# Optimization experiments

Measured on AMD Instinct MI355X. Metric: run time of the kernel, lower is better.

The kernel has to match this reference:

```python
import jax, jax.numpy as jnp
import numpy as np

EPS = 1e-12  # torch F.normalize eps

def setup_inputs() -> dict:
    key = jax.random.key(0)
    k1, k2 = jax.random.split(key)
    N, M, D = 256, 2000, 128
    gene_seq = jax.random.randint(k1, (N, M), 0, 4)
    embedding_mat = jax.random.normal(k2, (M, 4, D), dtype=jnp.float32) * (np.sqrt(2.0) / D)
    return {"gene_seq": gene_seq, "embedding_mat": embedding_mat}

def reference(gene_seq, embedding_mat):
    # L2-normalize each (gene, base) row along embedding dim (torch F.normalize semantics)
    norm = jnp.linalg.norm(embedding_mat, axis=-1, keepdims=True)
    table = embedding_mat / jnp.maximum(norm, EPS)  # (M, 4, D)
    M = table.shape[0]
    # One-hot einsum 'nmi,nmid->nmd' == direct gather of row gene_seq[n,m] at position m
    gene_idx = jnp.arange(M)[None, :]               # (1, M)
    out = table[gene_idx, gene_seq, :]              # (N, M, D)
    return out
```

## Files before the change

kernel.cpp:

```cpp
#include <hip/hip_runtime.h>


#define N_SEQ   256
#define M_GENES 2000
#define D_DIM   128
#define GENES_PER_BLOCK 8
#define N_CHUNK 64
#define GRID_X  (M_GENES / GENES_PER_BLOCK)
#define GRID_Y  (N_SEQ / N_CHUNK)

typedef float vfloat4 __attribute__((ext_vector_type(4)));

__global__ __launch_bounds__(256) void fused_gather_kernel(
    const int*   __restrict__ gene_seq,
    const float* __restrict__ emb,
    float*       __restrict__ out)
{
    const int tid  = threadIdx.x;
    const int wave = tid >> 6;
    const int lane = tid & 63;
    const int c    = lane & 31;

    const int m0    = blockIdx.x * GENES_PER_BLOCK;
    const int n0    = blockIdx.y * N_CHUNK;
    const int m_sel = m0 + (wave << 1) + (lane >> 5);

    vfloat4 r[4];
    #pragma unroll
    for (int g = 0; g < 4; ++g) {
        const vfloat4 v = *reinterpret_cast<const vfloat4*>(
            emb + (((m_sel << 2) + g) << 7) + (c << 2));
        float ss = v.x * v.x + v.y * v.y + v.z * v.z + v.w * v.w;
        ss += __shfl_xor(ss, 1, 32);
        ss += __shfl_xor(ss, 2, 32);
        ss += __shfl_xor(ss, 4, 32);
        ss += __shfl_xor(ss, 8, 32);
        ss += __shfl_xor(ss, 16, 32);
        const float inv = 1.0f / fmaxf(sqrtf(ss), 1e-12f);
        r[g] = v * inv;
    }

    const int g0 = gene_seq[(n0 + c)      * M_GENES + m_sel];
    const int g1 = gene_seq[(n0 + 32 + c) * M_GENES + m_sel];

    float* __restrict__ outbase = out + (size_t)(m_sel << 7) + (c << 2);

    #pragma unroll 4
    for (int n = 0; n < N_CHUNK; ++n) {
        const int src = (lane & 32) | (n & 31);
        const int gv  = __shfl((n < 32) ? g0 : g1, src, 64);

        const vfloat4 lo = (gv & 1) ? r[1] : r[0];
        const vfloat4 hi = (gv & 1) ? r[3] : r[2];
        const vfloat4 v  = (gv & 2) ? hi : lo;

        *reinterpret_cast<vfloat4*>(
            outbase + (size_t)(n0 + n) * (M_GENES * D_DIM)) = v;
    }
}

extern "C" void kernel_launch(void* const* d_in, const int* in_sizes, int n_in,
                              void* d_out, int out_size, void* d_ws, size_t ws_size,
                              hipStream_t stream) {
    const int*   gene_seq = (const int*)d_in[0];
    const float* emb      = (const float*)d_in[1];
    float*       out      = (float*)d_out;

    fused_gather_kernel<<<dim3(GRID_X, GRID_Y), dim3(256), 0, stream>>>(
        gene_seq, emb, out);
}
```

Measured before the change: 257.3 us.

## Stage normalized embedding tile and gene indices in LDS for gather

Each block now normalizes a 32-gene tile of embedding rows into shared memory and loads a 32x32 tile of gene indices with coalesced int2 reads. Output rows are then written from LDS using the index table, so each n-row writes 16KB contiguous spans per block instead of scattered 512B segments. It replaces register-held rows and per-element shuffles. In exchange it uses about 68KB of LDS per block, which limits occupancy, and it normalizes each embedding row once per n-chunk (8 times).

```diff
diff --git a/kernel.cpp b/kernel.cpp
--- a/kernel.cpp
+++ b/kernel.cpp
@@ -4,58 +4,82 @@
 #define N_SEQ   256
 #define M_GENES 2000
 #define D_DIM   128
-#define GENES_PER_BLOCK 8
-#define N_CHUNK 64
-#define GRID_X  (M_GENES / GENES_PER_BLOCK)
-#define GRID_Y  (N_SEQ / N_CHUNK)
+#define TILE_M  32
+#define N_TILES 63
+#define N_CHUNK 32
+#define NCH     (N_SEQ / N_CHUNK)
+#define THREADS 512
 
 typedef float vfloat4 __attribute__((ext_vector_type(4)));
 
-__global__ __launch_bounds__(256) void fused_gather_kernel(
+__global__ __launch_bounds__(THREADS) void gene_embed_kernel(
     const int*   __restrict__ gene_seq,
     const float* __restrict__ emb,
     float*       __restrict__ out)
 {
-    const int tid  = threadIdx.x;
-    const int wave = tid >> 6;
-    const int lane = tid & 63;
+    __shared__ float rowsN[TILE_M * 4 * D_DIM];
+    __shared__ int   gtab[N_CHUNK * TILE_M];
+
+    const int tile = blockIdx.x;
+    const int m0   = tile * TILE_M;
+    const int mv   = min(TILE_M, M_GENES - m0);
+    const int n0   = blockIdx.y * N_CHUNK;
+
+    const int t    = threadIdx.x;
+    const int w    = t >> 6;
+    const int lane = t & 63;
     const int c    = lane & 31;
+    const int half = lane >> 5;
 
-    const int m0    = blockIdx.x * GENES_PER_BLOCK;
-    const int n0    = blockIdx.y * N_CHUNK;
-    const int m_sel = m0 + (wave << 1) + (lane >> 5);
-
-    vfloat4 r[4];
-    #pragma unroll
-    for (int g = 0; g < 4; ++g) {
-        const vfloat4 v = *reinterpret_cast<const vfloat4*>(
-            emb + (((m_sel << 2) + g) << 7) + (c << 2));
-        float ss = v.x * v.x + v.y * v.y + v.z * v.z + v.w * v.w;
-        ss += __shfl_xor(ss, 1, 32);
-        ss += __shfl_xor(ss, 2, 32);
-        ss += __shfl_xor(ss, 4, 32);
-        ss += __shfl_xor(ss, 8, 32);
-        ss += __shfl_xor(ss, 16, 32);
-        const float inv = 1.0f / fmaxf(sqrtf(ss), 1e-12f);
-        r[g] = v * inv;
+    {
+        const float* embT = emb + (size_t)m0 * 4 * D_DIM;
+        const int R = mv * 4;
+        #pragma unroll
+        for (int it = 0; it < (TILE_M * 4) / 16; ++it) {
+            const int r = it * 16 + (w << 1) + half;
+            if (r < R) {
+                vfloat4 v = *reinterpret_cast<const vfloat4*>(embT + r * D_DIM + (c << 2));
+                float ss = v.x * v.x + v.y * v.y + v.z * v.z + v.w * v.w;
+                ss += __shfl_xor(ss, 1, 32);
+                ss += __shfl_xor(ss, 2, 32);
+                ss += __shfl_xor(ss, 4, 32);
+                ss += __shfl_xor(ss, 8, 32);
+                ss += __shfl_xor(ss, 16, 32);
+                const float inv = 1.0f / fmaxf(sqrtf(ss), 1e-12f);
+                v *= inv;
+                *reinterpret_cast<vfloat4*>(&rowsN[r * D_DIM + (c << 2)]) = v;
+            }
+        }
     }
 
-    const int g0 = gene_seq[(n0 + c)      * M_GENES + m_sel];
-    const int g1 = gene_seq[(n0 + 32 + c) * M_GENES + m_sel];
+    {
+        const int i   = t >> 4;
+        const int col = (t & 15) << 1;
+        long idx = (long)(n0 + i) * M_GENES + m0 + col;
+        const long maxi = (long)N_SEQ * M_GENES - 2;
+        if (idx > maxi) idx = maxi;
+        const int2 gv = *reinterpret_cast<const int2*>(gene_seq + idx);
+        *reinterpret_cast<int2*>(&gtab[(i << 5) + col]) = gv;
+    }
+    __syncthreads();
 
-    float* __restrict__ outbase = out + (size_t)(m_sel << 7) + (c << 2);
+    const int r0 = t >> 5;
+    const int cw = (t & 31) << 2;
+    float* base = out + (size_t)n0 * (M_GENES * D_DIM) + m0 * D_DIM + cw;
 
     #pragma unroll 4
     for (int n = 0; n < N_CHUNK; ++n) {
-        const int src = (lane & 32) | (n & 31);
-        const int gv  = __shfl((n < 32) ? g0 : g1, src, 64);
-
-        const vfloat4 lo = (gv & 1) ? r[1] : r[0];
-        const vfloat4 hi = (gv & 1) ? r[3] : r[2];
-        const vfloat4 v  = (gv & 2) ? hi : lo;
-
-        *reinterpret_cast<vfloat4*>(
-            outbase + (size_t)(n0 + n) * (M_GENES * D_DIM)) = v;
+        float* outn = base + (size_t)n * (M_GENES * D_DIM);
+        #pragma unroll
+        for (int j = 0; j < 2; ++j) {
+            const int gj = j * 16 + r0;
+            if (m0 + gj < M_GENES) {
+                const int g = gtab[(n << 5) + gj];
+                const vfloat4 v = *reinterpret_cast<const vfloat4*>(
+                    &rowsN[((gj << 2) + g) * D_DIM + cw]);
+                *reinterpret_cast<vfloat4*>(outn + (gj << 7)) = v;
+            }
+        }
     }
 }
 
@@ -66,6 +90,6 @@
     const float* emb      = (const float*)d_in[1];
     float*       out      = (float*)d_out;
 
-    fused_gather_kernel<<<dim3(GRID_X, GRID_Y), dim3(256), 0, stream>>>(
+    gene_embed_kernel<<<dim3(N_TILES, NCH), dim3(THREADS), 0, stream>>>(
         gene_seq, emb, out);
 }
```

Result: slower. 264.3 us (+2.7%).
